# Kernel tuning notes

Measured on AMD Instinct MI355X. Metric: run time of the kernel, lower is better.

## Reference

```python
import jax, jax.numpy as jnp
import numpy as np
import math

N_OFFSETS = 72
FMAP_H = 10
FMAP_W = 25
IMG_W = 800
STRIDE = 32


def _gen_anchor(start, angle_deg, ys):
    # anchor layout: [score0, score1, start_y(1-sy), start_x, length, xs...]
    a = np.zeros(5 + len(ys), np.float32)
    ang = math.radians(angle_deg)
    sx, sy = start
    a[2] = 1.0 - sy
    a[3] = sx
    a[5:] = (sx + (1.0 - ys - 1.0 + sy) / math.tan(ang)) * IMG_W
    return a


def _side(angles, nb, x=None, y=None):
    if x is None:
        starts = [(xx, 1.0) for xx in np.linspace(1.0, 0.0, nb)]
    else:
        starts = [(x, yy) for yy in np.linspace(1.0, 0.0, nb)]
    ys_full = np.linspace(1.0, 0.0, N_OFFSETS)
    ys_cut = np.linspace(1.0, 0.0, FMAP_H)
    A = np.stack([_gen_anchor(s, a, ys_full) for s in starts for a in angles])
    Ac = np.stack([_gen_anchor(s, a, ys_cut) for s in starts for a in angles])
    return A, Ac


def _build_anchors():
    left = _side([72., 60., 49., 39., 30., 22.], 72, x=0.0)
    right = _side([108., 120., 131., 141., 150., 158.], 72, x=1.0)
    bottom = _side([165., 150., 141., 131., 120., 108., 100., 90., 80., 72., 60., 49., 39., 30., 15.], 128, y=1.0)
    anchors = np.concatenate([left[0], bottom[0], right[0]]).astype(np.float32)  # (N, 5+72)
    cut = np.concatenate([left[1], bottom[1], right[1]])                          # (N, 5+Hf)
    unclamped = np.flip(np.round(cut[:, 5:] / STRIDE), axis=1).astype(np.int32)   # (N, Hf)
    cut_xs = np.clip(unclamped, 0, FMAP_W - 1).astype(np.int32)
    invalid = (unclamped < 0) | (unclamped > FMAP_W)
    return anchors, cut_xs, invalid


def setup_inputs() -> dict:
    key = jax.random.key(0)
    ks = jax.random.split(key, 10)
    B, C_IN, CF = 8, 512, 64
    anchors_np, cut_xs_np, invalid_np = _build_anchors()
    N = anchors_np.shape[0]  # 2784
    D = CF * FMAP_H          # 640
    s = 0.01
    return {
        "x": jax.random.normal(ks[0], (B, C_IN, FMAP_H, FMAP_W), jnp.float32),
        "conv_w": jax.random.normal(ks[1], (CF, C_IN), jnp.float32) * s,
        "conv_b": jnp.zeros((CF,), jnp.float32),
        "attn_w": jax.random.normal(ks[2], (N - 1, D), jnp.float32) * s,
        "attn_b": jnp.zeros((N - 1,), jnp.float32),
        "cls_w": jax.random.normal(ks[3], (2, 2 * D), jnp.float32) * s,
        "cls_b": jnp.zeros((2,), jnp.float32),
        "reg_w": jax.random.normal(ks[4], (N_OFFSETS + 1, 2 * D), jnp.float32) * s,
        "reg_b": jnp.zeros((N_OFFSETS + 1,), jnp.float32),
        "anchors": jnp.asarray(anchors_np),
        "cut_xs": jnp.asarray(cut_xs_np),
        "invalid_mask": jnp.asarray(invalid_np),
    }


def reference(x, conv_w, conv_b, attn_w, attn_b, cls_w, cls_b, reg_w, reg_b, anchors, cut_xs, invalid_mask):
    B = x.shape[0]
    N, Hf = cut_xs.shape
    Cf = conv_w.shape[0]
    # 1x1 conv
    feat = jnp.einsum('bchw,fc->bfhw', x, conv_w) + conv_b[None, :, None, None]
    # cut anchor features: gather irregular (v,u) columns -> (B, Cf, N, Hf)
    ys = jnp.arange(Hf)
    g = feat[:, :, ys[None, :], cut_xs]
    g = jnp.where(invalid_mask[None, None], jnp.zeros((), x.dtype), g)
    pf = g.transpose(0, 2, 1, 3).reshape(B, N, Cf * Hf)  # (B, N, D)
    # learned attention over anchors
    scores = jnp.einsum('bnd,md->bnm', pf, attn_w) + attn_b  # (B, N, N-1)
    attn = jax.nn.softmax(scores, axis=-1)
    # scatter into NxN matrix with zero diagonal (row i gets its N-1 values in off-diag cols)
    rows = jnp.arange(N)[:, None]
    cols = jnp.arange(N - 1)[None, :] + (jnp.arange(N - 1)[None, :] >= rows)
    attn_mat = jnp.zeros((B, N, N), x.dtype).at[:, rows, cols].set(attn)
    # aggregate features across anchors
    att_feats = jnp.einsum('bij,bjd->bid', attn_mat, pf)
    cat = jnp.concatenate([att_feats, pf], axis=-1)  # (B, N, 2D)
    cls_logits = jnp.einsum('bnd,cd->bnc', cat, cls_w) + cls_b
    reg = jnp.einsum('bnd,cd->bnc', cat, reg_w) + reg_b  # (B, N, n_offsets+1)
    lanes = jnp.broadcast_to(anchors[None], (B,) + anchors.shape)
    lanes = lanes.at[:, :, 4].set(reg[:, :, 0])
    lanes = lanes.at[:, :, 5:].add(reg[:, :, 1:])
    return cls_logits, lanes, attn_mat
```

## Files before the change

### kernel.cpp

```cpp
#include <hip/hip_runtime.h>

typedef unsigned short ushort_t;
typedef unsigned int   uint32;
typedef __attribute__((ext_vector_type(8))) short short8;
typedef __attribute__((ext_vector_type(4))) float f32x4;
typedef __attribute__((ext_vector_type(4))) uint32 u32x4;

#define B_     8
#define CIN    512
#define HFM    10
#define WFM    25
#define CF     64
#define NANCH  2784
#define NANCHP 2816
#define NM     2783
#define NMPAD  2816
#define D_     640
#define D2     1280
#define ALEN   77
#define M_     (B_*NANCH)
#define NO     128

#define VMCNT(N)   asm volatile("s_waitcnt vmcnt(" #N ")" ::: "memory")
#define S_BARRIER() do { __builtin_amdgcn_s_barrier(); __builtin_amdgcn_sched_barrier(0); } while (0)

__device__ __forceinline__ ushort_t f2bf(float f) {
    uint32 u = __float_as_uint(f);
    u += 0x7fffu + ((u >> 16) & 1u);
    return (ushort_t)(u >> 16);
}
__device__ __forceinline__ float bf2f(ushort_t h) {
    return __uint_as_float(((uint32)h) << 16);
}

__device__ __forceinline__ void gload16(const ushort_t* g, ushort_t* l) {
    __builtin_amdgcn_global_load_lds(
        (const __attribute__((address_space(1))) void*)g,
        (__attribute__((address_space(3))) void*)l, 16, 0, 0);
}

__global__ __launch_bounds__(256) void conv_feat_k(const float* __restrict__ x,
    const float* __restrict__ w, const float* __restrict__ bias,
    float* __restrict__ feat)
{
    int t = blockIdx.x * 256 + threadIdx.x;
    if (t >= B_ * CF * HFM * WFM) return;
    int pos = t % (HFM * WFM);
    int f   = (t / (HFM * WFM)) % CF;
    int b   = t / (CF * HFM * WFM);
    const float* xp = x + (size_t)b * CIN * HFM * WFM + pos;
    const float* wp = w + (size_t)f * CIN;
    float s = bias[f];
#pragma unroll 4
    for (int c = 0; c < CIN; ++c)
        s += xp[(size_t)c * (HFM * WFM)] * wp[c];
    feat[t] = s;
}

__global__ __launch_bounds__(256) void gather_pf_k(const float* __restrict__ feat,
    const int* __restrict__ cut_xs, const unsigned char* __restrict__ invalid,
    ushort_t* __restrict__ pf16)
{
    long long t = (long long)blockIdx.x * 256 + threadIdx.x;
    if (t >= (long long)M_ * D_) return;
    int d = (int)(t % D_);
    int r = (int)(t / D_);
    int n = r % NANCH;
    int b = r / NANCH;
    int f = d / HFM, h = d - f * HFM;
    int idx = n * HFM + h;
    float v = 0.f;
    if (!invalid[idx]) {
        int xs = cut_xs[idx];
        v = feat[((size_t)(b * CF + f) * HFM + h) * WFM + xs];
    }
    pf16[t] = f2bf(v);
}

__global__ __launch_bounds__(256) void prep_attn_w_k(const float* __restrict__ attn_w,
    ushort_t* __restrict__ w16)
{
    int t = blockIdx.x * 256 + threadIdx.x;
    if (t >= NMPAD * D_) return;
    int m = t / D_;
    w16[t] = (m < NM) ? f2bf(attn_w[(size_t)m * D_ + (t % D_)]) : (ushort_t)0;
}

__global__ __launch_bounds__(256) void prep_heads_w_k(const float* __restrict__ cls_w,
    const float* __restrict__ reg_w, ushort_t* __restrict__ w16)
{
    int t = blockIdx.x * 256 + threadIdx.x;
    if (t >= 128 * D2) return;
    int o = t / D2, k = t % D2;
    float v = 0.f;
    if (o < 2)       v = cls_w[(size_t)o * D2 + k];
    else if (o < 75) v = reg_w[(size_t)(o - 2) * D2 + k];
    w16[t] = (o < 75) ? f2bf(v) : (ushort_t)0;
}

__global__ __launch_bounds__(256) void zero_gtpad_k(ushort_t* __restrict__ Gt)
{
    int t = blockIdx.x * 256 + threadIdx.x;
    if (t >= B_ * NO * 32) return;
    int n = t & 31, o = (t >> 5) & (NO - 1), b = t >> 12;
    Gt[((size_t)b * NO + o) * NANCHP + NANCH + n] = 0;
}

__global__ __launch_bounds__(256) void zero_epad_k(ushort_t* __restrict__ E)
{
    int t = blockIdx.x * 256 + threadIdx.x;
    if (t < M_) {
        E[(size_t)t * NANCHP + (t % NANCH)] = 0;
    } else if (t < M_ * 17) {
        int idx = t - M_;
        int r = idx >> 4, w = idx & 15;
        *(uint32*)&E[(size_t)r * NANCHP + NANCH + 2 * w] = 0;
    }
}


__global__ __launch_bounds__(256, 4) void scores_mfma_k(
    const ushort_t* __restrict__ A,
    const ushort_t* __restrict__ Bw,
    const float* __restrict__ attn_b,
    ushort_t* __restrict__ E)
{
    __shared__ __align__(16) ushort_t As[2][4096];
    __shared__ __align__(16) ushort_t Bs[2][4096];
    const int orig = blockIdx.x;
    const int xcd = orig & 7, pos = orig >> 3;
    const int start = (xcd < 4) ? xcd * 479 : 1916 + (xcd - 4) * 478;
    const int idx = start + pos;
    const int rowb = idx / 22, colb = idx - rowb * 22;
    const int row0 = rowb * 128, col0 = colb * 128;
    const int t = threadIdx.x;
    const int wid = t >> 6, lane = t & 63;
    const int wr = wid >> 1, wc = wid & 1;
    const int srow = lane >> 2;
    const int swk  = (((lane & 3) ^ ((lane >> 3) & 3)) * 8);
    const ushort_t* gA = A  + (size_t)(row0 + wid * 32 + srow) * D_ + swk;
    const ushort_t* gB = Bw + (size_t)(col0 + wid * 32 + srow) * D_ + swk;
    f32x4 acc[4][4];
#pragma unroll
    for (int i = 0; i < 4; ++i)
#pragma unroll
        for (int j = 0; j < 4; ++j) acc[i][j] = (f32x4){0.f, 0.f, 0.f, 0.f};
    const int cl = lane & 15, q = lane >> 4;
    const int ra = wr * 64 + cl, rb = wc * 64 + cl;
    const int aoff = ra * 32 + ((q ^ ((ra >> 1) & 3)) * 8);
    const int boff = rb * 32 + ((q ^ ((rb >> 1) & 3)) * 8);

    auto STAGE = [&](int buf, int k0) {
        ushort_t* la = &As[buf][wid * 1024];
        ushort_t* lb = &Bs[buf][wid * 1024];
        gload16(gA + k0, la);
        gload16(gA + k0 + 16 * D_, la + 512);
        gload16(gB + k0, lb);
        gload16(gB + k0 + 16 * D_, lb + 512);
    };
    auto COMPUTE = [&](int buf) {
        short8 af[4], bv[4];
#pragma unroll
        for (int i = 0; i < 4; ++i) af[i] = *(const short8*)&As[buf][aoff + i * 512];
#pragma unroll
        for (int j = 0; j < 4; ++j) bv[j] = *(const short8*)&Bs[buf][boff + j * 512];
        __builtin_amdgcn_s_setprio(1);
#pragma unroll
        for (int i = 0; i < 4; ++i)
#pragma unroll
            for (int j = 0; j < 4; ++j)
                acc[i][j] = __builtin_amdgcn_mfma_f32_16x16x32_bf16(af[i], bv[j], acc[i][j], 0, 0, 0);
        __builtin_amdgcn_s_setprio(0);
    };

    const int NT = D_ / 32;
    STAGE(0, 0); STAGE(1, 32);
    int cur = 0;
    for (int tl = 0; tl < NT - 1; ++tl) {
        VMCNT(4); S_BARRIER();
        COMPUTE(cur);
        S_BARRIER();
        if (tl + 2 < NT) STAGE(cur, (tl + 2) * 32);
        cur ^= 1;
    }
    VMCNT(0); S_BARRIER();
    COMPUTE(cur);

#pragma unroll
    for (int i = 0; i < 4; ++i) {
#pragma unroll
        for (int ee = 0; ee < 4; ++ee) {
            int r = row0 + wr * 64 + i * 16 + q * 4 + ee;
            int n = r % NANCH;
            ushort_t* orow = E + (size_t)r * NANCHP;
#pragma unroll
            for (int j = 0; j < 4; ++j) {
                int m = col0 + wc * 64 + j * 16 + cl;
                if (m < NM) orow[m + (m >= n)] = f2bf(__expf(acc[i][j][ee] + attn_b[m]));
            }
        }
    }
}

__global__ __launch_bounds__(256) void normalize_k(const ushort_t* __restrict__ E,
    float* __restrict__ attn, float* __restrict__ rsum)
{
    const int r = blockIdx.x;
    float* row = attn + (size_t)r * NANCH;
    const ushort_t* row16 = E + (size_t)r * NANCHP;
    const int t = threadIdx.x;
    __shared__ float red[4];
    float vals[16];
    float s = 0.f;
#pragma unroll
    for (int i = 0; i < 2; ++i) {
        int c = t + i * 256;
        float v0 = 0.f, v1 = 0.f, v2 = 0.f, v3 = 0.f, v4 = 0.f, v5 = 0.f, v6 = 0.f, v7 = 0.f;
        if (c < 348) {
            u32x4 u = *(const u32x4*)&row16[8 * c];
            v0 = bf2f((ushort_t)(u.x & 0xffffu)); v1 = bf2f((ushort_t)(u.x >> 16));
            v2 = bf2f((ushort_t)(u.y & 0xffffu)); v3 = bf2f((ushort_t)(u.y >> 16));
            v4 = bf2f((ushort_t)(u.z & 0xffffu)); v5 = bf2f((ushort_t)(u.z >> 16));
            v6 = bf2f((ushort_t)(u.w & 0xffffu)); v7 = bf2f((ushort_t)(u.w >> 16));
        }
        vals[8 * i + 0] = v0; vals[8 * i + 1] = v1; vals[8 * i + 2] = v2; vals[8 * i + 3] = v3;
        vals[8 * i + 4] = v4; vals[8 * i + 5] = v5; vals[8 * i + 6] = v6; vals[8 * i + 7] = v7;
        s += ((v0 + v1) + (v2 + v3)) + ((v4 + v5) + (v6 + v7));
    }
    for (int off = 32; off; off >>= 1) s += __shfl_down(s, off);
    if ((t & 63) == 0) red[t >> 6] = s;
    __syncthreads();
    s = red[0] + red[1] + red[2] + red[3];
    float inv = 1.0f / s;
    if (t == 0) rsum[r] = s;
#pragma unroll
    for (int i = 0; i < 2; ++i) {
        int c = t + i * 256;
        if (c < 348) {
            float4 w0 = make_float4(vals[8 * i] * inv, vals[8 * i + 1] * inv,
                                    vals[8 * i + 2] * inv, vals[8 * i + 3] * inv);
            float4 w1 = make_float4(vals[8 * i + 4] * inv, vals[8 * i + 5] * inv,
                                    vals[8 * i + 6] * inv, vals[8 * i + 7] * inv);
            *(float4*)&row[8 * c]     = w0;
            *(float4*)&row[8 * c + 4] = w1;
        }
    }
}

__global__ __launch_bounds__(256, 2) void gx_mfma_k(
    const ushort_t* __restrict__ A,
    const ushort_t* __restrict__ W,
    ushort_t* __restrict__ Gt)
{
    __shared__ __align__(16) ushort_t As[2][8192];
    __shared__ __align__(16) ushort_t Bs[2][8192];
    const int t = threadIdx.x;
    const int wid = t >> 6, lane = t & 63;
    const int wr = wid >> 1, wc = wid & 1;
    const int row0 = blockIdx.x * 128;
    const int r8 = lane >> 3;
    const int ck = (lane & 7) ^ r8;
    const ushort_t* gA = A + (size_t)(row0 + wid * 8 + r8) * D_ + ck * 8;
    const ushort_t* gB = W + (size_t)(wid * 8 + r8) * D2 + ck * 8;
    f32x4 acc[4][4];
#pragma unroll
    for (int i = 0; i < 4; ++i)
#pragma unroll
        for (int j = 0; j < 4; ++j) acc[i][j] = (f32x4){0.f, 0.f, 0.f, 0.f};
    const int cl = lane & 15, q = lane >> 4, cl7 = lane & 7;

    auto STAGE = [&](int buf, int k0) {
        ushort_t* la = &As[buf][wid * 512];
        ushort_t* lb = &Bs[buf][wid * 512];
#pragma unroll
        for (int j = 0; j < 4; ++j) {
            gload16(gA + k0 + (size_t)j * 32 * D_, la + j * 2048);
            gload16(gB + k0 + (size_t)j * 32 * D2, lb + j * 2048);
        }
    };
    auto COMPUTE = [&](int buf) {
#pragma unroll
        for (int ks = 0; ks < 2; ++ks) {
            short8 af[4], bv[4];
            const int co = ((ks * 4 + q) ^ cl7) * 8;
#pragma unroll
            for (int i = 0; i < 4; ++i)
                af[i] = *(const short8*)&As[buf][(wr * 64 + i * 16 + cl) * 64 + co];
#pragma unroll
            for (int j = 0; j < 4; ++j)
                bv[j] = *(const short8*)&Bs[buf][(wc * 64 + j * 16 + cl) * 64 + co];
            __builtin_amdgcn_s_setprio(1);
#pragma unroll
            for (int i = 0; i < 4; ++i)
#pragma unroll
                for (int j = 0; j < 4; ++j)
                    acc[i][j] = __builtin_amdgcn_mfma_f32_16x16x32_bf16(af[i], bv[j], acc[i][j], 0, 0, 0);
            __builtin_amdgcn_s_setprio(0);
        }
    };

    const int NT = D_ / 64;
    STAGE(0, 0); STAGE(1, 64);
    int cur = 0;
    for (int tl = 0; tl < NT - 1; ++tl) {
        VMCNT(8); S_BARRIER();
        COMPUTE(cur);
        S_BARRIER();
        if (tl + 2 < NT) STAGE(cur, (tl + 2) * 64);
        cur ^= 1;
    }
    VMCNT(0); S_BARRIER();
    COMPUTE(cur);

#pragma unroll
    for (int i = 0; i < 4; ++i) {
#pragma unroll
        for (int ee = 0; ee < 4; ++ee) {
            int r = row0 + wr * 64 + i * 16 + q * 4 + ee;
            int b = r / NANCH, nl = r - b * NANCH;
#pragma unroll
            for (int j = 0; j < 4; ++j) {
                int o = wc * 64 + j * 16 + cl;
                Gt[((size_t)b * NO + o) * NANCHP + nl] = f2bf(acc[i][j][ee]);
            }
        }
    }
}

__global__ __launch_bounds__(256, 4) void final_mfma_k(
    const ushort_t* __restrict__ E16,
    const ushort_t* __restrict__ pf16,
    const ushort_t* __restrict__ Gt,
    const ushort_t* __restrict__ W,
    float* __restrict__ part)
{
    __shared__ __align__(16) ushort_t As[2][4096];
    __shared__ __align__(16) ushort_t Bs[2][4096];
    const int b = blockIdx.x & 7;
    const int u = blockIdx.x >> 3;
    const int rb = u % 22, kc = u / 22;
    const int g0 = (kc < 4) ? kc * 22 : 88;
    const int NT = (kc < 4) ? 22 : 20;
    const int t = threadIdx.x;
    const int wid = t >> 6, lane = t & 63;
    const int wr = wid >> 1, wc = wid & 1;
    const int srow = lane >> 2;
    const int swk  = (((lane & 3) ^ ((lane >> 3) & 3)) * 8);
    const size_t arow = (size_t)b * NANCH + rb * 128 + wid * 32 + srow;
    const ushort_t* gAa = E16  + arow * NANCHP + swk;
    const ushort_t* gAp = pf16 + arow * D_ + swk;
    const ushort_t* gBg = Gt + ((size_t)b * NO + wid * 32 + srow) * NANCHP + swk;
    const ushort_t* gBw = W + (size_t)(wid * 32 + srow) * D2 + D_ + swk;
    f32x4 acc[4][4];
#pragma unroll
    for (int i = 0; i < 4; ++i)
#pragma unroll
        for (int j = 0; j < 4; ++j) acc[i][j] = (f32x4){0.f, 0.f, 0.f, 0.f};
    const int cl = lane & 15, q = lane >> 4;
    const int ra = wr * 64 + cl, rbb = wc * 64 + cl;
    const int aoff = ra * 32 + ((q ^ ((ra >> 1) & 3)) * 8);
    const int boff = rbb * 32 + ((q ^ ((rbb >> 1) & 3)) * 8);

    auto STAGE = [&](int buf, int gt) {
        ushort_t* la = &As[buf][wid * 1024];
        ushort_t* lb = &Bs[buf][wid * 1024];
        if (gt < 88) {
            const int k0 = gt * 32;
            gload16(gAa + k0, la);
            gload16(gAa + k0 + (size_t)16 * NANCHP, la + 512);
            gload16(gBg + k0, lb);
            gload16(gBg + k0 + (size_t)16 * NANCHP, lb + 512);
        } else {
            const int kk = (gt - 88) * 32;
            gload16(gAp + kk, la);
            gload16(gAp + kk + (size_t)16 * D_, la + 512);
            gload16(gBw + kk, lb);
            gload16(gBw + kk + (size_t)16 * D2, lb + 512);
        }
    };
    auto COMPUTE = [&](int buf) {
        short8 af[4], bv[4];
#pragma unroll
        for (int i = 0; i < 4; ++i) af[i] = *(const short8*)&As[buf][aoff + i * 512];
#pragma unroll
        for (int j = 0; j < 4; ++j) bv[j] = *(const short8*)&Bs[buf][boff + j * 512];
        __builtin_amdgcn_s_setprio(1);
#pragma unroll
        for (int i = 0; i < 4; ++i)
#pragma unroll
            for (int j = 0; j < 4; ++j)
                acc[i][j] = __builtin_amdgcn_mfma_f32_16x16x32_bf16(af[i], bv[j], acc[i][j], 0, 0, 0);
        __builtin_amdgcn_s_setprio(0);
    };

    STAGE(0, g0); STAGE(1, g0 + 1);
    int cur = 0;
    for (int tl = 0; tl < NT - 1; ++tl) {
        VMCNT(4); S_BARRIER();
        COMPUTE(cur);
        S_BARRIER();
        if (tl + 2 < NT) STAGE(cur, g0 + tl + 2);
        cur ^= 1;
    }
    VMCNT(0); S_BARRIER();
    COMPUTE(cur);

    float* pout = part + (size_t)kc * M_ * NO;
#pragma unroll
    for (int i = 0; i < 4; ++i) {
#pragma unroll
        for (int ee = 0; ee < 4; ++ee) {
            int nl = rb * 128 + wr * 64 + i * 16 + q * 4 + ee;
            if (nl < NANCH) {
                int r = b * NANCH + nl;
#pragma unroll
                for (int j = 0; j < 4; ++j) {
                    int oo = wc * 64 + j * 16 + cl;
                    pout[(size_t)r * NO + oo] = acc[i][j][ee];
                }
            }
        }
    }
}

__global__ __launch_bounds__(256) void reduce_heads_k(
    const float* __restrict__ part,
    const float* __restrict__ rsum,
    const float* __restrict__ cls_b, const float* __restrict__ reg_b,
    const float* __restrict__ anchors,
    float* __restrict__ cls_out, float* __restrict__ lanes)
{
    int t = blockIdx.x * 256 + threadIdx.x;
    if (t >= M_ * 80) return;
    int r = t / 80, oo = t - r * 80;
    int nl = r % NANCH;
    if (oo < 75) {
        float inv = 1.0f / rsum[r];
        size_t base = (size_t)r * NO + oo, st = (size_t)M_ * NO;
        float v = ((part[base] + part[base + st]) + (part[base + 2 * st] + part[base + 3 * st])) * inv
                + part[base + 4 * st];
        if (oo < 2) {
            cls_out[(size_t)r * 2 + oo] = v + cls_b[oo];
        } else {
            int qq = oo - 2;
            int c = 4 + qq;
            float res = v + reg_b[qq];
            if (qq > 0) res += anchors[(size_t)nl * ALEN + c];
            lanes[(size_t)r * ALEN + c] = res;
        }
    } else if (oo < 79) {
        int c = oo - 75;
        lanes[(size_t)r * ALEN + c] = anchors[(size_t)nl * ALEN + c];
    }
}

extern "C" void kernel_launch(void* const* d_in, const int* in_sizes, int n_in,
                              void* d_out, int out_size, void* d_ws, size_t ws_size,
                              hipStream_t stream)
{
    (void)in_sizes; (void)n_in; (void)out_size; (void)ws_size;
    const float* x       = (const float*)d_in[0];
    const float* conv_w  = (const float*)d_in[1];
    const float* conv_b  = (const float*)d_in[2];
    const float* attn_w  = (const float*)d_in[3];
    const float* attn_b  = (const float*)d_in[4];
    const float* cls_w   = (const float*)d_in[5];
    const float* cls_b   = (const float*)d_in[6];
    const float* reg_w   = (const float*)d_in[7];
    const float* reg_b   = (const float*)d_in[8];
    const float* anchors = (const float*)d_in[9];
    const int*   cut_xs  = (const int*)d_in[10];
    const unsigned char* invalid = (const unsigned char*)d_in[11];

    float* out     = (float*)d_out;
    float* cls_out = out;
    float* lanes   = out + (size_t)M_ * 2;
    float* attn    = out + (size_t)M_ * 2 + (size_t)M_ * ALEN;

    char* w = (char*)d_ws;
    float* feat      = (float*)w;    w += (size_t)B_ * CF * HFM * WFM * 4;
    ushort_t* pf16   = (ushort_t*)w; w += (size_t)M_ * D_ * 2;
    ushort_t* aw16   = (ushort_t*)w; w += (size_t)NMPAD * D_ * 2;
    ushort_t* hw16   = (ushort_t*)w; w += (size_t)128 * D2 * 2;
    ushort_t* Gt     = (ushort_t*)w; w += (size_t)B_ * NO * NANCHP * 2;
    float* part      = (float*)w;    w += (size_t)5 * M_ * NO * 4;
    float* rsum      = (float*)w;    w += (size_t)M_ * 4;
    ushort_t* E16    = (ushort_t*)w; w += (size_t)(M_ + 32) * NANCHP * 2;

    conv_feat_k<<<(B_ * CF * HFM * WFM + 255) / 256, 256, 0, stream>>>(x, conv_w, conv_b, feat);
    gather_pf_k<<<(int)(((long long)M_ * D_ + 255) / 256), 256, 0, stream>>>(feat, cut_xs, invalid, pf16);
    prep_attn_w_k<<<(NMPAD * D_ + 255) / 256, 256, 0, stream>>>(attn_w, aw16);
    prep_heads_w_k<<<(128 * D2 + 255) / 256, 256, 0, stream>>>(cls_w, reg_w, hw16);

    gx_mfma_k<<<M_ / 128, 256, 0, stream>>>(pf16, hw16, Gt);
    zero_gtpad_k<<<(B_ * NO * 32 + 255) / 256, 256, 0, stream>>>(Gt);
    zero_epad_k<<<(M_ * 17 + 255) / 256, 256, 0, stream>>>(E16);

    scores_mfma_k<<<dim3(174 * 22), 256, 0, stream>>>(pf16, aw16, attn_b, E16);
    normalize_k<<<M_, 256, 0, stream>>>(E16, attn, rsum);

    final_mfma_k<<<dim3(5 * 22 * B_), 256, 0, stream>>>(E16, pf16, Gt, hw16, part);
    reduce_heads_k<<<(M_ * 80 + 255) / 256, 256, 0, stream>>>(part, rsum, cls_b, reg_b,
                                                              anchors, cls_out, lanes);
}
```

Measured before the change: 413.7 us.

## Replace LDS-staged MFMA GEMMs with direct global loads and fold E padding zeroing

Three MFMA GEMM kernels drop their double-buffered LDS staging through global_load_lds. Each lane now reads its bf16 fragments directly from global memory into registers, and the block barriers go away. The separate zero_epad kernel is removed: the scores kernel now writes zeros for the diagonal and the padding columns itself, saving one launch and a pass over memory. The cost is that each operand is reloaded per wave with no LDS reuse, and the loads are strided 16-byte reads, which may raise L2 traffic and latency stalls.

```diff
diff --git a/kernel.cpp b/kernel.cpp
--- a/kernel.cpp
+++ b/kernel.cpp
@@ -21,9 +21,6 @@
 #define M_     (B_*NANCH)
 #define NO     128
 
-#define VMCNT(N)   asm volatile("s_waitcnt vmcnt(" #N ")" ::: "memory")
-#define S_BARRIER() do { __builtin_amdgcn_s_barrier(); __builtin_amdgcn_sched_barrier(0); } while (0)
-
 __device__ __forceinline__ ushort_t f2bf(float f) {
     uint32 u = __float_as_uint(f);
     u += 0x7fffu + ((u >> 16) & 1u);
@@ -31,12 +28,6 @@
 }
 __device__ __forceinline__ float bf2f(ushort_t h) {
     return __uint_as_float(((uint32)h) << 16);
-}
-
-__device__ __forceinline__ void gload16(const ushort_t* g, ushort_t* l) {
-    __builtin_amdgcn_global_load_lds(
-        (const __attribute__((address_space(1))) void*)g,
-        (__attribute__((address_space(3))) void*)l, 16, 0, 0);
 }
 
 __global__ __launch_bounds__(256) void conv_feat_k(const float* __restrict__ x,
@@ -106,18 +97,6 @@
     Gt[((size_t)b * NO + o) * NANCHP + NANCH + n] = 0;
 }
 
-__global__ __launch_bounds__(256) void zero_epad_k(ushort_t* __restrict__ E)
-{
-    int t = blockIdx.x * 256 + threadIdx.x;
-    if (t < M_) {
-        E[(size_t)t * NANCHP + (t % NANCH)] = 0;
-    } else if (t < M_ * 17) {
-        int idx = t - M_;
-        int r = idx >> 4, w = idx & 15;
-        *(uint32*)&E[(size_t)r * NANCHP + NANCH + 2 * w] = 0;
-    }
-}
-
 
 __global__ __launch_bounds__(256, 4) void scores_mfma_k(
     const ushort_t* __restrict__ A,
@@ -125,8 +104,6 @@
     const float* __restrict__ attn_b,
     ushort_t* __restrict__ E)
 {
-    __shared__ __align__(16) ushort_t As[2][4096];
-    __shared__ __align__(16) ushort_t Bs[2][4096];
     const int orig = blockIdx.x;
     const int xcd = orig & 7, pos = orig >> 3;
     const int start = (xcd < 4) ? xcd * 479 : 1916 + (xcd - 4) * 478;
@@ -136,55 +113,33 @@
     const int t = threadIdx.x;
     const int wid = t >> 6, lane = t & 63;
     const int wr = wid >> 1, wc = wid & 1;
-    const int srow = lane >> 2;
-    const int swk  = (((lane & 3) ^ ((lane >> 3) & 3)) * 8);
-    const ushort_t* gA = A  + (size_t)(row0 + wid * 32 + srow) * D_ + swk;
-    const ushort_t* gB = Bw + (size_t)(col0 + wid * 32 + srow) * D_ + swk;
+    const int cl = lane & 15, q = lane >> 4;
+    const ushort_t* pa[4];
+    const ushort_t* pb[4];
+#pragma unroll
+    for (int i = 0; i < 4; ++i) {
+        pa[i] = A  + (size_t)(row0 + wr * 64 + i * 16 + cl) * D_ + q * 8;
+        pb[i] = Bw + (size_t)(col0 + wc * 64 + i * 16 + cl) * D_ + q * 8;
+    }
     f32x4 acc[4][4];
 #pragma unroll
     for (int i = 0; i < 4; ++i)
 #pragma unroll
         for (int j = 0; j < 4; ++j) acc[i][j] = (f32x4){0.f, 0.f, 0.f, 0.f};
-    const int cl = lane & 15, q = lane >> 4;
-    const int ra = wr * 64 + cl, rb = wc * 64 + cl;
-    const int aoff = ra * 32 + ((q ^ ((ra >> 1) & 3)) * 8);
-    const int boff = rb * 32 + ((q ^ ((rb >> 1) & 3)) * 8);
-
-    auto STAGE = [&](int buf, int k0) {
-        ushort_t* la = &As[buf][wid * 1024];
-        ushort_t* lb = &Bs[buf][wid * 1024];
-        gload16(gA + k0, la);
-        gload16(gA + k0 + 16 * D_, la + 512);
-        gload16(gB + k0, lb);
-        gload16(gB + k0 + 16 * D_, lb + 512);
-    };
-    auto COMPUTE = [&](int buf) {
+
+#pragma unroll 4
+    for (int k0 = 0; k0 < D_; k0 += 32) {
         short8 af[4], bv[4];
 #pragma unroll
-        for (int i = 0; i < 4; ++i) af[i] = *(const short8*)&As[buf][aoff + i * 512];
-#pragma unroll
-        for (int j = 0; j < 4; ++j) bv[j] = *(const short8*)&Bs[buf][boff + j * 512];
-        __builtin_amdgcn_s_setprio(1);
+        for (int i = 0; i < 4; ++i) af[i] = *(const short8*)(pa[i] + k0);
+#pragma unroll
+        for (int j = 0; j < 4; ++j) bv[j] = *(const short8*)(pb[j] + k0);
 #pragma unroll
         for (int i = 0; i < 4; ++i)
 #pragma unroll
             for (int j = 0; j < 4; ++j)
                 acc[i][j] = __builtin_amdgcn_mfma_f32_16x16x32_bf16(af[i], bv[j], acc[i][j], 0, 0, 0);
-        __builtin_amdgcn_s_setprio(0);
-    };
-
-    const int NT = D_ / 32;
-    STAGE(0, 0); STAGE(1, 32);
-    int cur = 0;
-    for (int tl = 0; tl < NT - 1; ++tl) {
-        VMCNT(4); S_BARRIER();
-        COMPUTE(cur);
-        S_BARRIER();
-        if (tl + 2 < NT) STAGE(cur, (tl + 2) * 32);
-        cur ^= 1;
-    }
-    VMCNT(0); S_BARRIER();
-    COMPUTE(cur);
+    }
 
 #pragma unroll
     for (int i = 0; i < 4; ++i) {
@@ -197,7 +152,10 @@
             for (int j = 0; j < 4; ++j) {
                 int m = col0 + wc * 64 + j * 16 + cl;
                 if (m < NM) orow[m + (m >= n)] = f2bf(__expf(acc[i][j][ee] + attn_b[m]));
+                else if (m < NMPAD - 1) orow[m + 1] = 0;
             }
+            int dc = n - (col0 + wc * 64);
+            if (dc >= 0 && dc < 64 && (dc & 15) == cl) orow[n] = 0;
         }
     }
 }
@@ -247,70 +205,42 @@
     }
 }
 
-__global__ __launch_bounds__(256, 2) void gx_mfma_k(
+__global__ __launch_bounds__(256, 4) void gx_mfma_k(
     const ushort_t* __restrict__ A,
     const ushort_t* __restrict__ W,
     ushort_t* __restrict__ Gt)
 {
-    __shared__ __align__(16) ushort_t As[2][8192];
-    __shared__ __align__(16) ushort_t Bs[2][8192];
+    const int row0 = blockIdx.x * 128;
     const int t = threadIdx.x;
     const int wid = t >> 6, lane = t & 63;
     const int wr = wid >> 1, wc = wid & 1;
-    const int row0 = blockIdx.x * 128;
-    const int r8 = lane >> 3;
-    const int ck = (lane & 7) ^ r8;
-    const ushort_t* gA = A + (size_t)(row0 + wid * 8 + r8) * D_ + ck * 8;
-    const ushort_t* gB = W + (size_t)(wid * 8 + r8) * D2 + ck * 8;
+    const int cl = lane & 15, q = lane >> 4;
+    const ushort_t* pa[4];
+    const ushort_t* pb[4];
+#pragma unroll
+    for (int i = 0; i < 4; ++i) {
+        pa[i] = A + (size_t)(row0 + wr * 64 + i * 16 + cl) * D_ + q * 8;
+        pb[i] = W + (size_t)(wc * 64 + i * 16 + cl) * D2 + q * 8;
+    }
     f32x4 acc[4][4];
 #pragma unroll
     for (int i = 0; i < 4; ++i)
 #pragma unroll
         for (int j = 0; j < 4; ++j) acc[i][j] = (f32x4){0.f, 0.f, 0.f, 0.f};
-    const int cl = lane & 15, q = lane >> 4, cl7 = lane & 7;
-
-    auto STAGE = [&](int buf, int k0) {
-        ushort_t* la = &As[buf][wid * 512];
-        ushort_t* lb = &Bs[buf][wid * 512];
-#pragma unroll
-        for (int j = 0; j < 4; ++j) {
-            gload16(gA + k0 + (size_t)j * 32 * D_, la + j * 2048);
-            gload16(gB + k0 + (size_t)j * 32 * D2, lb + j * 2048);
-        }
-    };
-    auto COMPUTE = [&](int buf) {
-#pragma unroll
-        for (int ks = 0; ks < 2; ++ks) {
-            short8 af[4], bv[4];
-            const int co = ((ks * 4 + q) ^ cl7) * 8;
-#pragma unroll
-            for (int i = 0; i < 4; ++i)
-                af[i] = *(const short8*)&As[buf][(wr * 64 + i * 16 + cl) * 64 + co];
+
+#pragma unroll 4
+    for (int k0 = 0; k0 < D_; k0 += 32) {
+        short8 af[4], bv[4];
+#pragma unroll
+        for (int i = 0; i < 4; ++i) af[i] = *(const short8*)(pa[i] + k0);
+#pragma unroll
+        for (int j = 0; j < 4; ++j) bv[j] = *(const short8*)(pb[j] + k0);
+#pragma unroll
+        for (int i = 0; i < 4; ++i)
 #pragma unroll
             for (int j = 0; j < 4; ++j)
-                bv[j] = *(const short8*)&Bs[buf][(wc * 64 + j * 16 + cl) * 64 + co];
-            __builtin_amdgcn_s_setprio(1);
-#pragma unroll
-            for (int i = 0; i < 4; ++i)
-#pragma unroll
-                for (int j = 0; j < 4; ++j)
-                    acc[i][j] = __builtin_amdgcn_mfma_f32_16x16x32_bf16(af[i], bv[j], acc[i][j], 0, 0, 0);
-            __builtin_amdgcn_s_setprio(0);
-        }
-    };
-
-    const int NT = D_ / 64;
-    STAGE(0, 0); STAGE(1, 64);
-    int cur = 0;
-    for (int tl = 0; tl < NT - 1; ++tl) {
-        VMCNT(8); S_BARRIER();
-        COMPUTE(cur);
-        S_BARRIER();
-        if (tl + 2 < NT) STAGE(cur, (tl + 2) * 64);
-        cur ^= 1;
-    }
-    VMCNT(0); S_BARRIER();
-    COMPUTE(cur);
+                acc[i][j] = __builtin_amdgcn_mfma_f32_16x16x32_bf16(af[i], bv[j], acc[i][j], 0, 0, 0);
+    }
 
 #pragma unroll
     for (int i = 0; i < 4; ++i) {
@@ -334,76 +264,63 @@
     const ushort_t* __restrict__ W,
     float* __restrict__ part)
 {
-    __shared__ __align__(16) ushort_t As[2][4096];
-    __shared__ __align__(16) ushort_t Bs[2][4096];
     const int b = blockIdx.x & 7;
     const int u = blockIdx.x >> 3;
     const int rb = u % 22, kc = u / 22;
-    const int g0 = (kc < 4) ? kc * 22 : 88;
-    const int NT = (kc < 4) ? 22 : 20;
     const int t = threadIdx.x;
     const int wid = t >> 6, lane = t & 63;
     const int wr = wid >> 1, wc = wid & 1;
-    const int srow = lane >> 2;
-    const int swk  = (((lane & 3) ^ ((lane >> 3) & 3)) * 8);
-    const size_t arow = (size_t)b * NANCH + rb * 128 + wid * 32 + srow;
-    const ushort_t* gAa = E16  + arow * NANCHP + swk;
-    const ushort_t* gAp = pf16 + arow * D_ + swk;
-    const ushort_t* gBg = Gt + ((size_t)b * NO + wid * 32 + srow) * NANCHP + swk;
-    const ushort_t* gBw = W + (size_t)(wid * 32 + srow) * D2 + D_ + swk;
+    const int cl = lane & 15, q = lane >> 4;
     f32x4 acc[4][4];
 #pragma unroll
     for (int i = 0; i < 4; ++i)
 #pragma unroll
         for (int j = 0; j < 4; ++j) acc[i][j] = (f32x4){0.f, 0.f, 0.f, 0.f};
-    const int cl = lane & 15, q = lane >> 4;
-    const int ra = wr * 64 + cl, rbb = wc * 64 + cl;
-    const int aoff = ra * 32 + ((q ^ ((ra >> 1) & 3)) * 8);
-    const int boff = rbb * 32 + ((q ^ ((rbb >> 1) & 3)) * 8);
-
-    auto STAGE = [&](int buf, int gt) {
-        ushort_t* la = &As[buf][wid * 1024];
-        ushort_t* lb = &Bs[buf][wid * 1024];
-        if (gt < 88) {
-            const int k0 = gt * 32;
-            gload16(gAa + k0, la);
-            gload16(gAa + k0 + (size_t)16 * NANCHP, la + 512);
-            gload16(gBg + k0, lb);
-            gload16(gBg + k0 + (size_t)16 * NANCHP, lb + 512);
-        } else {
-            const int kk = (gt - 88) * 32;
-            gload16(gAp + kk, la);
-            gload16(gAp + kk + (size_t)16 * D_, la + 512);
-            gload16(gBw + kk, lb);
-            gload16(gBw + kk + (size_t)16 * D2, lb + 512);
-        }
-    };
-    auto COMPUTE = [&](int buf) {
-        short8 af[4], bv[4];
-#pragma unroll
-        for (int i = 0; i < 4; ++i) af[i] = *(const short8*)&As[buf][aoff + i * 512];
-#pragma unroll
-        for (int j = 0; j < 4; ++j) bv[j] = *(const short8*)&Bs[buf][boff + j * 512];
-        __builtin_amdgcn_s_setprio(1);
-#pragma unroll
-        for (int i = 0; i < 4; ++i)
-#pragma unroll
-            for (int j = 0; j < 4; ++j)
-                acc[i][j] = __builtin_amdgcn_mfma_f32_16x16x32_bf16(af[i], bv[j], acc[i][j], 0, 0, 0);
-        __builtin_amdgcn_s_setprio(0);
-    };
-
-    STAGE(0, g0); STAGE(1, g0 + 1);
-    int cur = 0;
-    for (int tl = 0; tl < NT - 1; ++tl) {
-        VMCNT(4); S_BARRIER();
-        COMPUTE(cur);
-        S_BARRIER();
-        if (tl + 2 < NT) STAGE(cur, g0 + tl + 2);
-        cur ^= 1;
-    }
-    VMCNT(0); S_BARRIER();
-    COMPUTE(cur);
+
+    if (kc < 4) {
+        const int k0b = kc * 22 * 32;
+        const ushort_t* pa[4];
+        const ushort_t* pb[4];
+#pragma unroll
+        for (int i = 0; i < 4; ++i) {
+            pa[i] = E16 + ((size_t)b * NANCH + rb * 128 + wr * 64 + i * 16 + cl) * NANCHP + k0b + q * 8;
+            pb[i] = Gt  + ((size_t)b * NO + wc * 64 + i * 16 + cl) * NANCHP + k0b + q * 8;
+        }
+#pragma unroll 4
+        for (int k0 = 0; k0 < 22 * 32; k0 += 32) {
+            short8 af[4], bv[4];
+#pragma unroll
+            for (int i = 0; i < 4; ++i) af[i] = *(const short8*)(pa[i] + k0);
+#pragma unroll
+            for (int j = 0; j < 4; ++j) bv[j] = *(const short8*)(pb[j] + k0);
+#pragma unroll
+            for (int i = 0; i < 4; ++i)
+#pragma unroll
+                for (int j = 0; j < 4; ++j)
+                    acc[i][j] = __builtin_amdgcn_mfma_f32_16x16x32_bf16(af[i], bv[j], acc[i][j], 0, 0, 0);
+        }
+    } else {
+        const ushort_t* pa[4];
+        const ushort_t* pb[4];
+#pragma unroll
+        for (int i = 0; i < 4; ++i) {
+            pa[i] = pf16 + ((size_t)b * NANCH + rb * 128 + wr * 64 + i * 16 + cl) * D_ + q * 8;
+            pb[i] = W + (size_t)(wc * 64 + i * 16 + cl) * D2 + D_ + q * 8;
+        }
+#pragma unroll 4
+        for (int k0 = 0; k0 < D_; k0 += 32) {
+            short8 af[4], bv[4];
+#pragma unroll
+            for (int i = 0; i < 4; ++i) af[i] = *(const short8*)(pa[i] + k0);
+#pragma unroll
+            for (int j = 0; j < 4; ++j) bv[j] = *(const short8*)(pb[j] + k0);
+#pragma unroll
+            for (int i = 0; i < 4; ++i)
+#pragma unroll
+                for (int j = 0; j < 4; ++j)
+                    acc[i][j] = __builtin_amdgcn_mfma_f32_16x16x32_bf16(af[i], bv[j], acc[i][j], 0, 0, 0);
+        }
+    }
 
     float* pout = part + (size_t)kc * M_ * NO;
 #pragma unroll
@@ -494,7 +411,6 @@
 
     gx_mfma_k<<<M_ / 128, 256, 0, stream>>>(pf16, hw16, Gt);
     zero_gtpad_k<<<(B_ * NO * 32 + 255) / 256, 256, 0, stream>>>(Gt);
-    zero_epad_k<<<(M_ * 17 + 255) / 256, 256, 0, stream>>>(E16);
 
     scores_mfma_k<<<dim3(174 * 22), 256, 0, stream>>>(pf16, aw16, attn_b, E16);
     normalize_k<<<M_, 256, 0, stream>>>(E16, attn, rsum);
```

Measured after the change: 675.9 us. 1.63x slower.

## Give each wave private LDS tiles in scores GEMM to drop block barriers

Applied to the files above, without the earlier changes.

Each wave now loads its own 64-row A and 64-row B slices into a private LDS region, so the workgroup-wide barriers in the k-loop become per-wave vmcnt/lgkmcnt waits. This removes cross-wave synchronisation stalls, but each A and B tile is now loaded twice per block (two waves share each row or column group). That doubles global/L2 traffic and LDS use (64KB per block), so the launch bound drops from 4 to 2 blocks per SM and occupancy falls.

```diff
diff --git a/kernel.cpp b/kernel.cpp
--- a/kernel.cpp
+++ b/kernel.cpp
@@ -22,6 +22,8 @@
 #define NO     128
 
 #define VMCNT(N)   asm volatile("s_waitcnt vmcnt(" #N ")" ::: "memory")
+#define LGKMCNT0() do { asm volatile("s_waitcnt lgkmcnt(0)" ::: "memory"); \
+                        __builtin_amdgcn_sched_barrier(0); } while (0)
 #define S_BARRIER() do { __builtin_amdgcn_s_barrier(); __builtin_amdgcn_sched_barrier(0); } while (0)
 
 __device__ __forceinline__ ushort_t f2bf(float f) {
@@ -119,14 +121,13 @@
 }
 
 
-__global__ __launch_bounds__(256, 4) void scores_mfma_k(
+__global__ __launch_bounds__(256, 2) void scores_mfma_k(
     const ushort_t* __restrict__ A,
     const ushort_t* __restrict__ Bw,
     const float* __restrict__ attn_b,
     ushort_t* __restrict__ E)
 {
-    __shared__ __align__(16) ushort_t As[2][4096];
-    __shared__ __align__(16) ushort_t Bs[2][4096];
+    __shared__ __align__(16) ushort_t LB[4][2][4096];
     const int orig = blockIdx.x;
     const int xcd = orig & 7, pos = orig >> 3;
     const int start = (xcd < 4) ? xcd * 479 : 1916 + (xcd - 4) * 478;
@@ -136,34 +137,33 @@
     const int t = threadIdx.x;
     const int wid = t >> 6, lane = t & 63;
     const int wr = wid >> 1, wc = wid & 1;
+    const int cl = lane & 15, q = lane >> 4;
     const int srow = lane >> 2;
     const int swk  = (((lane & 3) ^ ((lane >> 3) & 3)) * 8);
-    const ushort_t* gA = A  + (size_t)(row0 + wid * 32 + srow) * D_ + swk;
-    const ushort_t* gB = Bw + (size_t)(col0 + wid * 32 + srow) * D_ + swk;
+    const ushort_t* gA = A  + (size_t)(row0 + wr * 64 + srow) * D_ + swk;
+    const ushort_t* gB = Bw + (size_t)(col0 + wc * 64 + srow) * D_ + swk;
     f32x4 acc[4][4];
 #pragma unroll
     for (int i = 0; i < 4; ++i)
 #pragma unroll
         for (int j = 0; j < 4; ++j) acc[i][j] = (f32x4){0.f, 0.f, 0.f, 0.f};
-    const int cl = lane & 15, q = lane >> 4;
-    const int ra = wr * 64 + cl, rb = wc * 64 + cl;
-    const int aoff = ra * 32 + ((q ^ ((ra >> 1) & 3)) * 8);
-    const int boff = rb * 32 + ((q ^ ((rb >> 1) & 3)) * 8);
+    const int co = ((q ^ ((cl >> 1) & 3)) * 8);
 
     auto STAGE = [&](int buf, int k0) {
-        ushort_t* la = &As[buf][wid * 1024];
-        ushort_t* lb = &Bs[buf][wid * 1024];
-        gload16(gA + k0, la);
-        gload16(gA + k0 + 16 * D_, la + 512);
-        gload16(gB + k0, lb);
-        gload16(gB + k0 + 16 * D_, lb + 512);
+        ushort_t* pA = &LB[wid][buf][0];
+        ushort_t* pB = &LB[wid][buf][2048];
+#pragma unroll
+        for (int j = 0; j < 4; ++j) {
+            gload16(gA + k0 + (size_t)(j * 16) * D_, pA + j * 512);
+            gload16(gB + k0 + (size_t)(j * 16) * D_, pB + j * 512);
+        }
     };
     auto COMPUTE = [&](int buf) {
         short8 af[4], bv[4];
 #pragma unroll
-        for (int i = 0; i < 4; ++i) af[i] = *(const short8*)&As[buf][aoff + i * 512];
-#pragma unroll
-        for (int j = 0; j < 4; ++j) bv[j] = *(const short8*)&Bs[buf][boff + j * 512];
+        for (int i = 0; i < 4; ++i) af[i] = *(const short8*)&LB[wid][buf][(i * 16 + cl) * 32 + co];
+#pragma unroll
+        for (int j = 0; j < 4; ++j) bv[j] = *(const short8*)&LB[wid][buf][2048 + (j * 16 + cl) * 32 + co];
         __builtin_amdgcn_s_setprio(1);
 #pragma unroll
         for (int i = 0; i < 4; ++i)
@@ -177,13 +177,13 @@
     STAGE(0, 0); STAGE(1, 32);
     int cur = 0;
     for (int tl = 0; tl < NT - 1; ++tl) {
-        VMCNT(4); S_BARRIER();
+        VMCNT(8);
         COMPUTE(cur);
-        S_BARRIER();
+        LGKMCNT0();
         if (tl + 2 < NT) STAGE(cur, (tl + 2) * 32);
         cur ^= 1;
     }
-    VMCNT(0); S_BARRIER();
+    VMCNT(0);
     COMPUTE(cur);
 
 #pragma unroll
```

New measurement: 477.5 us. +15.4%, slower.
